# Kernel optimization log

Measured on AMD Instinct MI355X. Metric: run time of the kernel, lower is better.

The kernel has to match this reference:

```python
import jax, jax.numpy as jnp
import numpy as np

D_MODEL = 1024
N_HEADS = 16
HEAD_DIM = D_MODEL // N_HEADS


def setup_inputs() -> dict:
    key = jax.random.key(0)
    ks = jax.random.split(key, 5)
    B, T = 4, 2048
    x = jax.random.normal(ks[0], (B, T, D_MODEL), dtype=jnp.float32)
    s = 1.0 / np.sqrt(D_MODEL)
    W_qkv = jax.random.normal(ks[1], (D_MODEL, 3 * D_MODEL), dtype=jnp.float32) * s
    b_qkv = jnp.zeros((3 * D_MODEL,), dtype=jnp.float32)
    W_out = jax.random.normal(ks[2], (D_MODEL, D_MODEL), dtype=jnp.float32) * s
    b_out = jnp.zeros((D_MODEL,), dtype=jnp.float32)
    return {"x": x, "W_qkv": W_qkv, "b_qkv": b_qkv, "W_out": W_out, "b_out": b_out}


def reference(x, W_qkv, b_qkv, W_out, b_out):
    B, T, C = x.shape
    qkv = x @ W_qkv + b_qkv                      # [B,T,3C]
    q, k, v = jnp.split(qkv, 3, axis=-1)
    # [B,T,H,Dh] -> [B,H,T,Dh]
    q = q.reshape(B, T, N_HEADS, HEAD_DIM).transpose(0, 2, 1, 3)
    k = k.reshape(B, T, N_HEADS, HEAD_DIM).transpose(0, 2, 1, 3)
    v = v.reshape(B, T, N_HEADS, HEAD_DIM).transpose(0, 2, 1, 3)
    scale = HEAD_DIM ** -0.5
    attn = jnp.einsum('bhqd,bhkd->bhqk', q, k) * scale
    causal = jnp.triu(jnp.ones((T, T), dtype=bool), k=1)
    attn = jnp.where(causal, -jnp.inf, attn)
    attn = jax.nn.softmax(attn, axis=-1)
    out = jnp.einsum('bhqk,bhkd->bhqd', attn, v)
    out = out.transpose(0, 2, 1, 3).reshape(B, T, C)
    return out @ W_out + b_out
```

## Files before the change

### kernel.cpp

```cpp
#include <hip/hip_runtime.h>
#include <hip/hip_bf16.h>


typedef unsigned short u16;
typedef __attribute__((ext_vector_type(8))) short short8;
typedef __attribute__((ext_vector_type(4))) float f32x4;

#define N_HEADS 16
#define HEAD_DIM 64
#define TSEQ 2048
#define BATCH 4
#define MROWS (BATCH * TSEQ)
#define N3 3072

__device__ __forceinline__ void cp16(const u16* g, u16* l) {
  __builtin_amdgcn_global_load_lds((const __attribute__((address_space(1))) void*)g,
                                   (__attribute__((address_space(3))) void*)l, 16, 0, 0);
}

__device__ __forceinline__ f32x4 mfma16(short8 a, short8 b, f32x4 c) {
  return __builtin_amdgcn_mfma_f32_16x16x32_bf16(a, b, c, 0, 0, 0);
}

__device__ __forceinline__ u16 f2b(float f) {
  __hip_bfloat16 h = __float2bfloat16(f);
  return *reinterpret_cast<u16*>(&h);
}

__global__ __launch_bounds__(256) void cvt_f32_bf16(const float* __restrict__ src,
                                                    u16* __restrict__ dst, int n4) {
  int i = blockIdx.x * 256 + threadIdx.x;
  if (i < n4) {
    float4 v = *(const float4*)(src + (size_t)i * 4);
    u16* d = dst + (size_t)i * 4;
    d[0] = f2b(v.x); d[1] = f2b(v.y); d[2] = f2b(v.z); d[3] = f2b(v.w);
  }
}

__global__ void transpose_cvt(const float* __restrict__ src, u16* __restrict__ dst,
                              int R, int Cn) {
  __shared__ float tile[32][33];
  int c0 = blockIdx.x * 32, r0 = blockIdx.y * 32;
  for (int i = threadIdx.y; i < 32; i += 8)
    tile[i][threadIdx.x] = src[(size_t)(r0 + i) * Cn + c0 + threadIdx.x];
  __syncthreads();
  for (int i = threadIdx.y; i < 32; i += 8)
    dst[(size_t)(c0 + i) * R + r0 + threadIdx.x] = f2b(tile[threadIdx.x][i]);
}

__device__ __forceinline__ void gemm128_core(const u16* __restrict__ A,
                                             const u16* __restrict__ Bt,
                                             int m0, int n0,
                                             u16* Asm, u16* Bsm,
                                             f32x4 acc[4][4]) {
  const int tid = threadIdx.x;
  const int w = tid >> 6;
  const int lane = tid & 63;
  const int quad = lane >> 4;
  const int l16 = lane & 15;
  const int wm = (w >> 1) * 64;
  const int wn = (w & 1) * 64;

#pragma unroll
  for (int i = 0; i < 4; ++i)
#pragma unroll
    for (int j = 0; j < 4; ++j) acc[i][j] = (f32x4){0.f, 0.f, 0.f, 0.f};

#define STG128(k0_, b_)                                                     \
  do {                                                                      \
    _Pragma("unroll")                                                       \
    for (int p = 0; p < 2; ++p) {                                           \
      int s = p * 256 + tid;                                                \
      int row = s >> 2;                                                     \
      int c4 = (s & 3) ^ ((row >> 1) & 3);                                  \
      cp16(A + (size_t)(m0 + row) * 1024 + (k0_) + c4 * 8,                  \
           Asm + (size_t)(b_) * 4096 + (p * 256 + w * 64) * 8);             \
      cp16(Bt + (size_t)(n0 + row) * 1024 + (k0_) + c4 * 8,                 \
           Bsm + (size_t)(b_) * 4096 + (p * 256 + w * 64) * 8);             \
    }                                                                       \
  } while (0)

  STG128(0, 0);
  STG128(32, 1);
  asm volatile("s_waitcnt vmcnt(4)" ::: "memory");
  asm volatile("s_barrier" ::: "memory");

  for (int kt = 0; kt < 32; ++kt) {
    const u16* Ab = Asm + (kt & 1) * 4096;
    const u16* Bb = Bsm + (kt & 1) * 4096;
    short8 a[4], b[4];
#pragma unroll
    for (int i = 0; i < 4; ++i) {
      int row = wm + i * 16 + l16;
      int c4 = quad ^ ((row >> 1) & 3);
      a[i] = *(const short8*)(Ab + row * 32 + c4 * 8);
    }
#pragma unroll
    for (int j = 0; j < 4; ++j) {
      int row = wn + j * 16 + l16;
      int c4 = quad ^ ((row >> 1) & 3);
      b[j] = *(const short8*)(Bb + row * 32 + c4 * 8);
    }
    __builtin_amdgcn_s_setprio(1);
#pragma unroll
    for (int i = 0; i < 4; ++i)
#pragma unroll
      for (int j = 0; j < 4; ++j)
        acc[i][j] = mfma16(a[i], b[j], acc[i][j]);
    __builtin_amdgcn_s_setprio(0);

    asm volatile("s_barrier" ::: "memory");
    if (kt + 2 < 32) {
      STG128((kt + 2) * 32, kt & 1);
      asm volatile("s_waitcnt vmcnt(4)" ::: "memory");
    } else if (kt + 1 < 32) {
      asm volatile("s_waitcnt vmcnt(0)" ::: "memory");
    }
    asm volatile("s_barrier" ::: "memory");
  }
#undef STG128
}

__global__ __launch_bounds__(256) void gemm_qkv_kernel(
    const u16* __restrict__ x, const u16* __restrict__ Wt,
    const float* __restrict__ bias,
    u16* __restrict__ qb, u16* __restrict__ kb, u16* __restrict__ vtb) {
  __shared__ __align__(16) u16 Asm[2 * 4096];
  __shared__ __align__(16) u16 Bsm[2 * 4096];
  f32x4 acc[4][4];
  const int m0 = blockIdx.y * 128;
  const int n0 = blockIdx.x * 128;
  gemm128_core(x, Wt, m0, n0, Asm, Bsm, acc);

  const int tid = threadIdx.x;
  const int w = tid >> 6, lane = tid & 63, quad = lane >> 4, l16 = lane & 15;
  const int wm = (w >> 1) * 64, wn = (w & 1) * 64;
#pragma unroll
  for (int j = 0; j < 4; ++j) {
    int col = n0 + wn + j * 16 + l16;
    float bv = bias[col];
    int which = col >> 10;
    int rem = col & 1023;
    int h = rem >> 6, d = rem & 63;
#pragma unroll
    for (int i = 0; i < 4; ++i) {
#pragma unroll
      for (int r = 0; r < 4; ++r) {
        int m = m0 + wm + i * 16 + quad * 4 + r;
        int b_ = m >> 11, t = m & 2047;
        int bh = b_ * N_HEADS + h;
        u16 o = f2b(acc[i][j][r] + bv);
        if (which == 0)
          qb[((size_t)(bh * TSEQ + t) << 6) + d] = o;
        else if (which == 1)
          kb[((size_t)(bh * TSEQ + t) << 6) + d] = o;
        else
          vtb[((size_t)((bh << 6) + d)) * TSEQ + t] = o;
      }
    }
  }
}

__global__ __launch_bounds__(256, 5) void attn_kernel(const u16* __restrict__ qb,
                                                      const u16* __restrict__ kb,
                                                      const u16* __restrict__ vtb,
                                                      u16* __restrict__ ob) {
  const int qt = (TSEQ / 128 - 1) - blockIdx.x;
  const int bh = blockIdx.y;
  __shared__ __align__(16) u16 Ksm[2][4096];
  __shared__ __align__(16) u16 Vsm[2][4096];
  const int tid = threadIdx.x;
  const int w = tid >> 6, lane = tid & 63, quad = lane >> 4, l16 = lane & 15;
  const int qbase = qt * 128;

  short8 qf[2][2];
#pragma unroll
  for (int mi = 0; mi < 2; ++mi) {
    const u16* qr = qb + ((size_t)(bh * TSEQ + qbase + mi * 64 + w * 16 + l16)) * 64;
    qf[mi][0] = *(const short8*)(qr + quad * 8);
    qf[mi][1] = *(const short8*)(qr + 32 + quad * 8);
  }

  f32x4 o[2][4];
  float lp[2] = {0.f, 0.f};
#pragma unroll
  for (int mi = 0; mi < 2; ++mi)
#pragma unroll
    for (int j = 0; j < 4; ++j) o[mi][j] = (f32x4){0.f, 0.f, 0.f, 0.f};
  const float cexp = 0.18033688011112042f;
  const float M = 10.0f;

  const u16* kb_bh = kb + (size_t)bh * TSEQ * 64;
  const u16* vt_bh = vtb + (size_t)bh * 64 * TSEQ;
  const int nk = 2 * qt + 2;

#define STAGE(kt_, b_)                                                        \
  do {                                                                        \
    const u16* kbase_ = kb_bh + (size_t)((kt_) * 64) * 64;                    \
    const u16* vbase_ = vt_bh + (kt_) * 64;                                   \
    _Pragma("unroll")                                                         \
    for (int p = 0; p < 2; ++p) {                                             \
      int s_ = p * 256 + tid;                                                 \
      int row_ = s_ >> 3;                                                     \
      int c8_ = (s_ & 7) ^ (row_ & 7);                                        \
      int krow_ = (row_ & 0x23) | ((row_ & 0x0C) << 1) | ((row_ & 0x10) >> 2);\
      cp16(kbase_ + krow_ * 64 + c8_ * 8, &Ksm[b_][(p * 256 + w * 64) * 8]);  \
      cp16(vbase_ + (size_t)row_ * TSEQ + c8_ * 8,                            \
           &Vsm[b_][(p * 256 + w * 64) * 8]);                                 \
    }                                                                         \
  } while (0)

  STAGE(0, 0);

  for (int kt = 0; kt < nk; ++kt) {
    asm volatile("s_barrier" ::: "memory");
    if (kt + 1 < nk) {
      STAGE(kt + 1, (kt + 1) & 1);
      asm volatile("s_waitcnt vmcnt(4)" ::: "memory");
    } else {
      asm volatile("s_waitcnt vmcnt(0)" ::: "memory");
    }
    asm volatile("s_barrier" ::: "memory");

    const u16* Kb = Ksm[kt & 1];
    const u16* Vb = Vsm[kt & 1];

#pragma unroll
    for (int mi = 0; mi < 2; ++mi) {
      const int qmin = qbase + mi * 64 + w * 16;
      if (kt * 64 > qmin + 15) continue;
      const int qlane = qmin + l16;

      f32x4 s[4];
#pragma unroll
      for (int j = 0; j < 4; ++j) {
        int row = j * 16 + l16;
        int ca = quad ^ (row & 7);
        int cb = (4 + quad) ^ (row & 7);
        short8 k0 = *(const short8*)(Kb + row * 64 + ca * 8);
        short8 k1 = *(const short8*)(Kb + row * 64 + cb * 8);
        f32x4 z = (f32x4){0.f, 0.f, 0.f, 0.f};
        z = mfma16(k0, qf[mi][0], z);
        z = mfma16(k1, qf[mi][1], z);
        s[j] = z;
      }
      if (kt * 64 + 63 > qmin) {
#pragma unroll
        for (int j = 0; j < 4; ++j) {
#pragma unroll
          for (int r = 0; r < 4; ++r) {
            int kabs = kt * 64 + ((j >> 1) << 5) + (quad << 3) + ((j & 1) << 2) + r;
            if (kabs > qlane) s[j][r] = -1e30f;
          }
        }
      }
      short8 ap0, ap1;
#pragma unroll
      for (int j = 0; j < 4; ++j) {
#pragma unroll
        for (int r = 0; r < 4; ++r) {
          float p_ = __builtin_amdgcn_exp2f(__builtin_fmaf(s[j][r], cexp, -M));
          lp[mi] += p_;
          u16 pb = f2b(p_);
          if (j < 2) ap0[j * 4 + r] = (short)pb;
          else       ap1[(j - 2) * 4 + r] = (short)pb;
        }
      }
#pragma unroll
      for (int j = 0; j < 4; ++j) {
        int row = j * 16 + l16;
        int ca = quad ^ (row & 7);
        int cb = (4 + quad) ^ (row & 7);
        short8 v0 = *(const short8*)(Vb + row * 64 + ca * 8);
        short8 v1 = *(const short8*)(Vb + row * 64 + cb * 8);
        o[mi][j] = mfma16(ap0, v0, o[mi][j]);
        o[mi][j] = mfma16(ap1, v1, o[mi][j]);
      }
    }
  }
#undef STAGE

#pragma unroll
  for (int mi = 0; mi < 2; ++mi) {
    lp[mi] += __shfl_xor(lp[mi], 16);
    lp[mi] += __shfl_xor(lp[mi], 32);
  }
  const int b_ = bh >> 4, h = bh & 15;
#pragma unroll
  for (int mi = 0; mi < 2; ++mi) {
    float dn[4];
#pragma unroll
    for (int r = 0; r < 4; ++r)
      dn[r] = __shfl(lp[mi], (lane & 48) + quad * 4 + r);
#pragma unroll
    for (int j = 0; j < 4; ++j)
#pragma unroll
      for (int r = 0; r < 4; ++r) {
        int t = qbase + mi * 64 + w * 16 + quad * 4 + r;
        int d = j * 16 + l16;
        ob[((size_t)(b_ * TSEQ + t)) * 1024 + h * 64 + d] =
            f2b(o[mi][j][r] / dn[r]);
      }
  }
}

__global__ __launch_bounds__(256) void gemm_out_kernel(
    const u16* __restrict__ attn, const u16* __restrict__ Wt,
    const float* __restrict__ bias, float* __restrict__ out) {
  __shared__ __align__(16) u16 Asm[2 * 4096];
  __shared__ __align__(16) u16 Bsm[2 * 4096];
  f32x4 acc[4][4];
  const int m0 = blockIdx.y * 128;
  const int n0 = blockIdx.x * 128;
  gemm128_core(attn, Wt, m0, n0, Asm, Bsm, acc);

  const int tid = threadIdx.x;
  const int w = tid >> 6, lane = tid & 63, quad = lane >> 4, l16 = lane & 15;
  const int wm = (w >> 1) * 64, wn = (w & 1) * 64;
#pragma unroll
  for (int j = 0; j < 4; ++j) {
    int col = n0 + wn + j * 16 + l16;
    float bv = bias[col];
#pragma unroll
    for (int i = 0; i < 4; ++i)
#pragma unroll
      for (int r = 0; r < 4; ++r) {
        int m = m0 + wm + i * 16 + quad * 4 + r;
        out[(size_t)m * 1024 + col] = acc[i][j][r] + bv;
      }
  }
}

extern "C" void kernel_launch(void* const* d_in, const int* in_sizes, int n_in,
                              void* d_out, int out_size, void* d_ws, size_t ws_size,
                              hipStream_t stream) {
  const float* x    = (const float*)d_in[0];
  const float* Wqkv = (const float*)d_in[1];
  const float* bqkv = (const float*)d_in[2];
  const float* Wout = (const float*)d_in[3];
  const float* bout = (const float*)d_in[4];
  float* out = (float*)d_out;

  u16* ws = (u16*)d_ws;
  u16* xb     = ws;
  u16* wqkv_t = xb + (size_t)MROWS * 1024;
  u16* wout_t = wqkv_t + (size_t)N3 * 1024;
  u16* qbuf   = wout_t + (size_t)1024 * 1024;
  u16* kbuf   = qbuf + (size_t)MROWS * 1024;
  u16* vtbuf  = kbuf + (size_t)MROWS * 1024;
  u16* obuf   = vtbuf + (size_t)MROWS * 1024;
  (void)ws_size; (void)n_in; (void)in_sizes; (void)out_size;

  int n4 = MROWS * 1024 / 4;
  cvt_f32_bf16<<<(n4 + 255) / 256, 256, 0, stream>>>(x, xb, n4);
  transpose_cvt<<<dim3(N3 / 32, 1024 / 32), dim3(32, 8), 0, stream>>>(Wqkv, wqkv_t, 1024, N3);
  transpose_cvt<<<dim3(1024 / 32, 1024 / 32), dim3(32, 8), 0, stream>>>(Wout, wout_t, 1024, 1024);
  gemm_qkv_kernel<<<dim3(N3 / 128, MROWS / 128), 256, 0, stream>>>(xb, wqkv_t, bqkv, qbuf, kbuf, vtbuf);
  attn_kernel<<<dim3(TSEQ / 128, BATCH * N_HEADS), 256, 0, stream>>>(qbuf, kbuf, vtbuf, obuf);
  gemm_out_kernel<<<dim3(1024 / 128, MROWS / 128), 256, 0, stream>>>(obuf, wout_t, bout, out);
}
```

Baseline: 294.9 us.

## Fuse prep kernels and use unpipelined single-buffer GEMM for QKV projection

The three preprocessing launches (x conversion and two weight transposes) are merged into one prep kernel that dispatches on block index, saving launch overhead. The QKV GEMM now uses a simple single-buffered loop with two syncthreads per K step, halving its LDS use and possibly raising occupancy. The output GEMM keeps the double-buffered pipeline but no longer raises wave priority around the MFMA block. The QKV GEMM gives up load/compute overlap in exchange for the smaller LDS footprint.

```diff
diff --git a/kernel.cpp b/kernel.cpp
--- a/kernel.cpp
+++ b/kernel.cpp
@@ -27,28 +27,99 @@
   return *reinterpret_cast<u16*>(&h);
 }
 
-__global__ __launch_bounds__(256) void cvt_f32_bf16(const float* __restrict__ src,
-                                                    u16* __restrict__ dst, int n4) {
-  int i = blockIdx.x * 256 + threadIdx.x;
-  if (i < n4) {
-    float4 v = *(const float4*)(src + (size_t)i * 4);
-    u16* d = dst + (size_t)i * 4;
+#define PREP_CVT_BLOCKS 8192
+#define PREP_WQKV_BLOCKS (96 * 32)
+#define PREP_WOUT_BLOCKS (32 * 32)
+#define PREP_TOTAL (PREP_CVT_BLOCKS + PREP_WQKV_BLOCKS + PREP_WOUT_BLOCKS)
+
+__device__ __forceinline__ void transpose_tile(const float* __restrict__ src,
+                                               u16* __restrict__ dst,
+                                               int R, int Cn, int c0, int r0,
+                                               float (*tile)[33]) {
+  const int tx = threadIdx.x & 31, ty = threadIdx.x >> 5;
+  for (int i = ty; i < 32; i += 8)
+    tile[i][tx] = src[(size_t)(r0 + i) * Cn + c0 + tx];
+  __syncthreads();
+  for (int i = ty; i < 32; i += 8)
+    dst[(size_t)(c0 + i) * R + r0 + tx] = f2b(tile[tx][i]);
+}
+
+__global__ __launch_bounds__(256) void prep_kernel(
+    const float* __restrict__ x, u16* __restrict__ xb,
+    const float* __restrict__ Wqkv, u16* __restrict__ wqkv_t,
+    const float* __restrict__ Wout, u16* __restrict__ wout_t) {
+  __shared__ float tile[32][33];
+  const int bx = blockIdx.x;
+  if (bx < PREP_CVT_BLOCKS) {
+    int i = bx * 256 + threadIdx.x;
+    float4 v = *(const float4*)(x + (size_t)i * 4);
+    u16* d = xb + (size_t)i * 4;
     d[0] = f2b(v.x); d[1] = f2b(v.y); d[2] = f2b(v.z); d[3] = f2b(v.w);
-  }
-}
-
-__global__ void transpose_cvt(const float* __restrict__ src, u16* __restrict__ dst,
-                              int R, int Cn) {
-  __shared__ float tile[32][33];
-  int c0 = blockIdx.x * 32, r0 = blockIdx.y * 32;
-  for (int i = threadIdx.y; i < 32; i += 8)
-    tile[i][threadIdx.x] = src[(size_t)(r0 + i) * Cn + c0 + threadIdx.x];
-  __syncthreads();
-  for (int i = threadIdx.y; i < 32; i += 8)
-    dst[(size_t)(c0 + i) * R + r0 + threadIdx.x] = f2b(tile[threadIdx.x][i]);
-}
-
-__device__ __forceinline__ void gemm128_core(const u16* __restrict__ A,
+  } else if (bx < PREP_CVT_BLOCKS + PREP_WQKV_BLOCKS) {
+    int b2 = bx - PREP_CVT_BLOCKS;
+    int c0 = (b2 % 96) * 32, r0 = (b2 / 96) * 32;
+    transpose_tile(Wqkv, wqkv_t, 1024, N3, c0, r0, tile);
+  } else {
+    int b3 = bx - PREP_CVT_BLOCKS - PREP_WQKV_BLOCKS;
+    int c0 = (b3 % 32) * 32, r0 = (b3 / 32) * 32;
+    transpose_tile(Wout, wout_t, 1024, 1024, c0, r0, tile);
+  }
+}
+
+__device__ __forceinline__ void gemm128_sync(const u16* __restrict__ A,
+                                             const u16* __restrict__ Bt,
+                                             int m0, int n0,
+                                             u16* Asm, u16* Bsm,
+                                             f32x4 acc[4][4]) {
+  const int tid = threadIdx.x;
+  const int w = tid >> 6;
+  const int lane = tid & 63;
+  const int quad = lane >> 4;
+  const int l16 = lane & 15;
+  const int wm = (w >> 1) * 64;
+  const int wn = (w & 1) * 64;
+
+#pragma unroll
+  for (int i = 0; i < 4; ++i)
+#pragma unroll
+    for (int j = 0; j < 4; ++j) acc[i][j] = (f32x4){0.f, 0.f, 0.f, 0.f};
+
+  for (int k0 = 0; k0 < 1024; k0 += 32) {
+    __syncthreads();
+#pragma unroll
+    for (int p = 0; p < 2; ++p) {
+      int s = p * 256 + tid;
+      int row = s >> 2;
+      int c4 = (s & 3) ^ ((row >> 1) & 3);
+      cp16(A + (size_t)(m0 + row) * 1024 + k0 + c4 * 8,
+           Asm + (size_t)(p * 256 + w * 64) * 8);
+      cp16(Bt + (size_t)(n0 + row) * 1024 + k0 + c4 * 8,
+           Bsm + (size_t)(p * 256 + w * 64) * 8);
+    }
+    __syncthreads();
+
+    short8 a[4], b[4];
+#pragma unroll
+    for (int i = 0; i < 4; ++i) {
+      int row = wm + i * 16 + l16;
+      int c4 = quad ^ ((row >> 1) & 3);
+      a[i] = *(const short8*)(Asm + row * 32 + c4 * 8);
+    }
+#pragma unroll
+    for (int j = 0; j < 4; ++j) {
+      int row = wn + j * 16 + l16;
+      int c4 = quad ^ ((row >> 1) & 3);
+      b[j] = *(const short8*)(Bsm + row * 32 + c4 * 8);
+    }
+#pragma unroll
+    for (int i = 0; i < 4; ++i)
+#pragma unroll
+      for (int j = 0; j < 4; ++j)
+        acc[i][j] = mfma16(a[i], b[j], acc[i][j]);
+  }
+}
+
+__device__ __forceinline__ void gemm128_pipe(const u16* __restrict__ A,
                                              const u16* __restrict__ Bt,
                                              int m0, int n0,
                                              u16* Asm, u16* Bsm,
@@ -101,13 +172,11 @@
       int c4 = quad ^ ((row >> 1) & 3);
       b[j] = *(const short8*)(Bb + row * 32 + c4 * 8);
     }
-    __builtin_amdgcn_s_setprio(1);
 #pragma unroll
     for (int i = 0; i < 4; ++i)
 #pragma unroll
       for (int j = 0; j < 4; ++j)
         acc[i][j] = mfma16(a[i], b[j], acc[i][j]);
-    __builtin_amdgcn_s_setprio(0);
 
     asm volatile("s_barrier" ::: "memory");
     if (kt + 2 < 32) {
@@ -125,12 +194,12 @@
     const u16* __restrict__ x, const u16* __restrict__ Wt,
     const float* __restrict__ bias,
     u16* __restrict__ qb, u16* __restrict__ kb, u16* __restrict__ vtb) {
-  __shared__ __align__(16) u16 Asm[2 * 4096];
-  __shared__ __align__(16) u16 Bsm[2 * 4096];
+  __shared__ __align__(16) u16 Asm[128 * 32];
+  __shared__ __align__(16) u16 Bsm[128 * 32];
   f32x4 acc[4][4];
   const int m0 = blockIdx.y * 128;
   const int n0 = blockIdx.x * 128;
-  gemm128_core(x, Wt, m0, n0, Asm, Bsm, acc);
+  gemm128_sync(x, Wt, m0, n0, Asm, Bsm, acc);
 
   const int tid = threadIdx.x;
   const int w = tid >> 6, lane = tid & 63, quad = lane >> 4, l16 = lane & 15;
@@ -312,7 +381,7 @@
   f32x4 acc[4][4];
   const int m0 = blockIdx.y * 128;
   const int n0 = blockIdx.x * 128;
-  gemm128_core(attn, Wt, m0, n0, Asm, Bsm, acc);
+  gemm128_pipe(attn, Wt, m0, n0, Asm, Bsm, acc);
 
   const int tid = threadIdx.x;
   const int w = tid >> 6, lane = tid & 63, quad = lane >> 4, l16 = lane & 15;
@@ -351,10 +420,7 @@
   u16* obuf   = vtbuf + (size_t)MROWS * 1024;
   (void)ws_size; (void)n_in; (void)in_sizes; (void)out_size;
 
-  int n4 = MROWS * 1024 / 4;
-  cvt_f32_bf16<<<(n4 + 255) / 256, 256, 0, stream>>>(x, xb, n4);
-  transpose_cvt<<<dim3(N3 / 32, 1024 / 32), dim3(32, 8), 0, stream>>>(Wqkv, wqkv_t, 1024, N3);
-  transpose_cvt<<<dim3(1024 / 32, 1024 / 32), dim3(32, 8), 0, stream>>>(Wout, wout_t, 1024, 1024);
+  prep_kernel<<<PREP_TOTAL, 256, 0, stream>>>(x, xb, Wqkv, wqkv_t, Wout, wout_t);
   gemm_qkv_kernel<<<dim3(N3 / 128, MROWS / 128), 256, 0, stream>>>(xb, wqkv_t, bqkv, qbuf, kbuf, vtbuf);
   attn_kernel<<<dim3(TSEQ / 128, BATCH * N_HEADS), 256, 0, stream>>>(qbuf, kbuf, vtbuf, obuf);
   gemm_out_kernel<<<dim3(1024 / 128, MROWS / 128), 256, 0, stream>>>(obuf, wout_t, bout, out);
```

Result: no change. 293.6 us (-0.4%).
